# Kernel tuning notes

Hardware: AMD Instinct MI355X
Metric: run time of the kernel (lower is better)

The kernel has to match this reference:

```python
import jax, jax.numpy as jnp
import numpy as np

K = 3            # kernel_size
PAD = (K - 1) // 2
UM = 2           # um_dim
C_IN = 128
C_OUT = 128
SLOPE = 0.01     # F.leaky_relu default negative slope


def setup_inputs() -> dict:
    key = jax.random.key(0)
    k1, k2, k3 = jax.random.split(key, 3)
    xx = jax.random.normal(k1, (16, C_IN, 64, 64), dtype=jnp.float32)
    # Conv2d(C_in, C_out, K, stride=K, bias=True) parameters
    w = jax.random.normal(k2, (C_OUT, C_IN, K, K), dtype=jnp.float32) * 0.05
    b = jax.random.normal(k3, (C_OUT,), dtype=jnp.float32) * 0.05
    return {"xx": xx, "w": w, "b": b}


def reference(xx, w, b):
    B, C, H, Wd = xx.shape
    # --- unfold: replicate pad, then extract all KxK patches (stride 1) ---
    xp = jnp.pad(xx, ((0, 0), (0, 0), (PAD, PAD), (PAD, PAD)), mode="edge")
    # patches[b, c, r, s, i, j] = xp[b, c, i + r, j + s]   -> [B, C, K, K, H, W]
    patches = jnp.stack(
        [jnp.stack([xp[:, :, r:r + H, s:s + Wd] for s in range(K)], axis=2)
         for r in range(K)], axis=2)
    # --- subtract per-(um-slot, pixel) mean over channel groups and KxK ---
    g = patches.reshape(B, C // UM, UM, K, K, H, Wd)
    avgs = g.mean(axis=(1, 3, 4), keepdims=True)        # [B,1,UM,1,1,H,W]
    g = g - avgs
    p = g.reshape(B, C, K, K, H, Wd)
    # --- patch-wise conv (kernel_size == stride on the tiled image). The
    # torch code's transpose(2,4).transpose(-1,-2) tiling places patch col
    # offset s along tiled rows and row offset r along tiled cols, so the
    # conv weight w[o,c,r,s] pairs with patches[b,c,s,r,i,j]. ---
    out = jnp.einsum("ocrs,bcsrij->boij", w, p) + b[None, :, None, None]
    # leaky_relu
    out = jnp.where(out > 0, out, SLOPE * out)
    # --- add mean back per um-slot ---
    m = avgs[:, :, :, 0, 0]                             # [B,1,UM,H,W]
    O = out.shape[1]
    out = out.reshape(B, O // UM, UM, H, Wd) + m
    return out.reshape(B, O, H, Wd)
```

## Files before the change

kernel.cpp:

```cpp
#include <hip/hip_runtime.h>
#include <hip/hip_bf16.h>

typedef __bf16 bf16x8 __attribute__((ext_vector_type(8)));
typedef float  f32x4  __attribute__((ext_vector_type(4)));

#define NB 16
#define CI 128
#define CO 128
#define HH 64
#define WW 64

#define SROWS 4
#define SCOLS 66
#define SSTR  72

__global__ void prep(const float* __restrict__ w, __bf16* __restrict__ Ag,
                     float* __restrict__ wsum) {
    __shared__ float red[8];
    const int blk = blockIdx.x, tid = threadIdx.x;
    if (blk < 72) {
        int gid  = blk * 256 + tid;
        int l    = gid & 63;
        int frag = gid >> 6;
        int mt   = frag & 7;
        int t    = frag >> 3;
        int tap  = t >> 2;
        int r    = tap % 3;
        int s    = tap / 3;
        int o    = mt * 16 + (l & 15);
        int cb   = (t & 3) * 32 + (l >> 4) * 8;
        bf16x8 v;
        #pragma unroll
        for (int j = 0; j < 8; ++j)
            v[j] = (__bf16)w[((o * CI + cb + j) * 3 + r) * 3 + s];
        *(bf16x8*)(Ag + (size_t)gid * 8) = v;
    } else {
        int o = blk - 72;
        const float* p = w + (size_t)o * CI * 9;
        float se = 0.f, so = 0.f;
        for (int idx = tid; idx < CI * 9; idx += 256) {
            int c = idx / 9;
            float v = p[idx];
            if (c & 1) so += v; else se += v;
        }
        #pragma unroll
        for (int off = 32; off; off >>= 1) {
            se += __shfl_down(se, off);
            so += __shfl_down(so, off);
        }
        int wave = tid >> 6, lane = tid & 63;
        if (lane == 0) { red[wave * 2] = se; red[wave * 2 + 1] = so; }
        __syncthreads();
        if (tid == 0) {
            wsum[o]      = red[0] + red[2] + red[4] + red[6];
            wsum[CO + o] = red[1] + red[3] + red[5] + red[7];
        }
    }
}

__global__ __launch_bounds__(512, 4) void conv_main(
        const float* __restrict__ x,
        const float* __restrict__ bias,
        const float* __restrict__ wsum,
        const __bf16* __restrict__ Ag,
        float* __restrict__ out)
{
    __shared__ __align__(16) __bf16 slab[SROWS * SCOLS * SSTR];
    __shared__ float Srow[SROWS * SCOLS * 2];
    __shared__ float avgl[2 * 64 * 2];

    const int tid  = threadIdx.x;
    const int b    = blockIdx.y;
    const int row0 = blockIdx.x * 2;

    const float* xb = x + (size_t)b * CI * HH * WW;

    const int wave = tid >> 6, lane = tid & 63;
    const int wm = wave >> 1, wn = wave & 1;
    const int m = lane & 15, q = lane >> 4;

    f32x4 acc[2][4];
    #pragma unroll
    for (int i = 0; i < 2; ++i)
        #pragma unroll
        for (int j = 0; j < 4; ++j)
            acc[i][j] = (f32x4){0.f, 0.f, 0.f, 0.f};

    int bbase[4];
    #pragma unroll
    for (int nt = 0; nt < 4; ++nt)
        bbase[nt] = (wn * SCOLS + nt * 16 + m) * SSTR + q * 8;

    const __bf16* Aw = Ag + (size_t)(wm * 2) * 512 + (size_t)lane * 8;

    for (int half = 0; half < 2; ++half) {
        if (half) __syncthreads();
        for (int u = tid; u < SROWS * SCOLS * 8; u += 512) {
            int col = u % SCOLS;
            int rc  = u / SCOLS;
            int cg  = rc & 7;
            int r   = rc >> 3;
            int yi  = row0 - 1 + r; yi = yi < 0 ? 0 : (yi > HH - 1 ? HH - 1 : yi);
            int xi  = col - 1;      xi = xi < 0 ? 0 : (xi > WW - 1 ? WW - 1 : xi);
            const float* src = xb + (size_t)(half * 64 + cg * 8) * (HH * WW)
                                  + yi * WW + xi;
            bf16x8 v;
            #pragma unroll
            for (int j = 0; j < 8; ++j)
                v[j] = (__bf16)src[(size_t)j * (HH * WW)];
            *(bf16x8*)(slab + (r * SCOLS + col) * SSTR + cg * 8) = v;
        }
        __syncthreads();
        for (int u = tid; u < SROWS * SCOLS; u += 512) {
            const __bf16* p = slab + u * SSTR;
            float se = 0.f, so = 0.f;
            #pragma unroll
            for (int cg = 0; cg < 8; ++cg) {
                bf16x8 v = *(const bf16x8*)(p + cg * 8);
                se += (float)v[0] + (float)v[2] + (float)v[4] + (float)v[6];
                so += (float)v[1] + (float)v[3] + (float)v[5] + (float)v[7];
            }
            if (half) { se += Srow[u * 2 + 0]; so += Srow[u * 2 + 1]; }
            Srow[u * 2 + 0] = se;
            Srow[u * 2 + 1] = so;
        }
        __syncthreads();
        if (half == 1) {
            if (tid < 256) {
                int uu  = tid & 1;
                int col = (tid >> 1) & 63;
                int rr  = tid >> 7;
                float ssum = 0.f;
                #pragma unroll
                for (int dy = 0; dy < 3; ++dy)
                    #pragma unroll
                    for (int dx = 0; dx < 3; ++dx)
                        ssum += Srow[(((rr + dy) * SCOLS) + (col + dx)) * 2 + uu];
                avgl[tid] = ssum * (1.0f / 576.0f);
            }
            __syncthreads();
        }
        #pragma unroll
        for (int tap = 0; tap < 9; ++tap) {
            const int s_ = tap / 3, r3 = tap % 3;
            const int boff0 = (s_ * SCOLS + r3) * SSTR;
            #pragma unroll
            for (int cc = 0; cc < 2; ++cc) {
                const int t    = tap * 4 + half * 2 + cc;
                const int boff = boff0 + cc * 32;
                bf16x8 bfrag[4];
                #pragma unroll
                for (int nt = 0; nt < 4; ++nt)
                    bfrag[nt] = *(const bf16x8*)(slab + bbase[nt] + boff);
                bf16x8 afrag[2];
                #pragma unroll
                for (int i = 0; i < 2; ++i)
                    afrag[i] = *(const bf16x8*)(Aw + (size_t)t * 4096 + i * 512);
                #pragma unroll
                for (int i = 0; i < 2; ++i)
                    #pragma unroll
                    for (int nt = 0; nt < 4; ++nt)
                        acc[i][nt] = __builtin_amdgcn_mfma_f32_16x16x32_bf16(
                            afrag[i], bfrag[nt], acc[i][nt], 0, 0, 0);
            }
        }
    }

    float a0v[4], a1v[4];
    #pragma unroll
    for (int nt = 0; nt < 4; ++nt) {
        int col = nt * 16 + m;
        a0v[nt] = avgl[(wn * 64 + col) * 2 + 0];
        a1v[nt] = avgl[(wn * 64 + col) * 2 + 1];
    }
    float* outb = out + (size_t)b * CO * HH * WW + (size_t)(row0 + wn) * WW;
    #pragma unroll
    for (int i = 0; i < 2; ++i) {
        #pragma unroll
        for (int rg = 0; rg < 4; ++rg) {
            int o = wm * 32 + i * 16 + q * 4 + rg;
            float bo = bias[o];
            float w0 = wsum[o];
            float w1 = wsum[CO + o];
            float* po = outb + (size_t)o * (HH * WW);
            #pragma unroll
            for (int nt = 0; nt < 4; ++nt) {
                float v = acc[i][nt][rg] + bo - a0v[nt] * w0 - a1v[nt] * w1;
                v = v > 0.f ? v : 0.01f * v;
                v += (o & 1) ? a1v[nt] : a0v[nt];
                po[nt * 16 + m] = v;
            }
        }
    }
}

extern "C" void kernel_launch(void* const* d_in, const int* in_sizes, int n_in,
                              void* d_out, int out_size, void* d_ws, size_t ws_size,
                              hipStream_t stream) {
    const float* x    = (const float*)d_in[0];
    const float* w    = (const float*)d_in[1];
    const float* bias = (const float*)d_in[2];
    float* out = (float*)d_out;

    __bf16* Ag   = (__bf16*)d_ws;
    float*  wsum = (float*)((char*)d_ws + 294912);

    prep<<<200, 256, 0, stream>>>(w, Ag, wsum);

    dim3 grid(HH / 2, NB);
    conv_main<<<grid, 512, 0, stream>>>(x, bias, wsum, Ag, out);
}
```

Measured before the change: 104.6 us.

## Pre-transpose input to channel-quartered bf16, stage weights in LDS with async loads

```diff
diff --git a/kernel.cpp b/kernel.cpp
--- a/kernel.cpp
+++ b/kernel.cpp
@@ -10,16 +10,51 @@
 #define HH 64
 #define WW 64
 
-#define SROWS 4
 #define SCOLS 66
-#define SSTR  72
-
-__global__ void prep(const float* __restrict__ w, __bf16* __restrict__ Ag,
-                     float* __restrict__ wsum) {
+#define SPIX  (6 * SCOLS)
+#define QSZ   ((size_t)NB * HH * WW * 32)
+
+#define GLDS16(gp, lp) __builtin_amdgcn_global_load_lds( \
+    (const __attribute__((address_space(1))) unsigned int*)(const void*)(gp), \
+    (__attribute__((address_space(3))) unsigned int*)(void*)(lp), 16, 0, 0)
+
+__global__ void prep(const float* __restrict__ x, const float* __restrict__ w,
+                     __bf16* __restrict__ Ag, float* __restrict__ wsum,
+                     __bf16* __restrict__ xT, float* __restrict__ S) {
+    __shared__ float tile[128 * 65];
     __shared__ float red[8];
     const int blk = blockIdx.x, tid = threadIdx.x;
-    if (blk < 72) {
-        int gid  = blk * 256 + tid;
+    if (blk < 1024) {
+        const int bb = blk >> 6, y = blk & 63;
+        const float* xr = x + ((size_t)bb * CI) * (HH * WW) + y * WW;
+        for (int idx = tid; idx < 2048; idx += 256) {
+            int c = idx >> 4, x4 = idx & 15;
+            float4 v = *(const float4*)(xr + (size_t)c * (HH * WW) + x4 * 4);
+            *(float4*)(tile + c * 65 + x4 * 4) = v;
+        }
+        __syncthreads();
+        for (int idx = tid; idx < 1024; idx += 256) {
+            int px = idx >> 4, cg = idx & 15;
+            bf16x8 o8;
+            #pragma unroll
+            for (int j = 0; j < 8; ++j)
+                o8[j] = (__bf16)tile[(cg * 8 + j) * 65 + px];
+            __bf16* dst = xT + (size_t)(cg >> 2) * QSZ
+                        + (((size_t)bb * 64 + y) * 64 + px) * 32 + (cg & 3) * 8;
+            *(bf16x8*)dst = o8;
+        }
+        if (tid < 64) {
+            float se = 0.f, so = 0.f;
+            #pragma unroll 8
+            for (int c = 0; c < 128; c += 2) {
+                se += tile[c * 65 + tid];
+                so += tile[(c + 1) * 65 + tid];
+            }
+            float2 v = {se, so};
+            *(float2*)(S + (((size_t)bb * 64 + y) * 64 + tid) * 2) = v;
+        }
+    } else if (blk < 1096) {
+        int gid  = (blk - 1024) * 256 + tid;
         int l    = gid & 63;
         int frag = gid >> 6;
         int mt   = frag & 7;
@@ -35,7 +70,7 @@
             v[j] = (__bf16)w[((o * CI + cb + j) * 3 + r) * 3 + s];
         *(bf16x8*)(Ag + (size_t)gid * 8) = v;
     } else {
-        int o = blk - 72;
+        int o = blk - 1096;
         const float* p = w + (size_t)o * CI * 9;
         float se = 0.f, so = 0.f;
         for (int idx = tid; idx < CI * 9; idx += 256) {
@@ -48,8 +83,8 @@
             se += __shfl_down(se, off);
             so += __shfl_down(so, off);
         }
-        int wave = tid >> 6, lane = tid & 63;
-        if (lane == 0) { red[wave * 2] = se; red[wave * 2 + 1] = so; }
+        int wv = tid >> 6, lane = tid & 63;
+        if (lane == 0) { red[wv * 2] = se; red[wv * 2 + 1] = so; }
         __syncthreads();
         if (tid == 0) {
             wsum[o]      = red[0] + red[2] + red[4] + red[6];
@@ -58,30 +93,74 @@
     }
 }
 
-__global__ __launch_bounds__(512, 4) void conv_main(
-        const float* __restrict__ x,
+__global__ __launch_bounds__(512, 2) void conv_main(
+        const __bf16* __restrict__ xT,
+        const float* __restrict__ S,
         const float* __restrict__ bias,
         const float* __restrict__ wsum,
         const __bf16* __restrict__ Ag,
         float* __restrict__ out)
 {
-    __shared__ __align__(16) __bf16 slab[SROWS * SCOLS * SSTR];
-    __shared__ float Srow[SROWS * SCOLS * 2];
-    __shared__ float avgl[2 * 64 * 2];
+    __shared__ __align__(16) __bf16 Alds[9 * 4096];
+    __shared__ __align__(16) __bf16 slab[2][SPIX * 32];
+    __shared__ float SrowS[6 * 64 * 2];
+    __shared__ float avgl[512];
 
     const int tid  = threadIdx.x;
     const int b    = blockIdx.y;
-    const int row0 = blockIdx.x * 2;
-
-    const float* xb = x + (size_t)b * CI * HH * WW;
+    const int row0 = blockIdx.x * 4;
 
     const int wave = tid >> 6, lane = tid & 63;
-    const int wm = wave >> 1, wn = wave & 1;
-    const int m = lane & 15, q = lane >> 4;
-
-    f32x4 acc[2][4];
-    #pragma unroll
-    for (int i = 0; i < 2; ++i)
+    const int wm = wave >> 2;
+    const int wn = wave & 3;
+    const int m = lane & 15, qv = lane >> 4;
+
+    auto issue_A = [&](int qn, int a0, int a1) {
+        for (int a = a0 + wave; a < a1; a += 8) {
+            int tap = a >> 3, part = a & 7;
+            const __bf16* gp = Ag
+                + (((size_t)((tap * 4 + qn) * 8 + part)) << 9) + (lane << 3);
+            GLDS16(gp, &Alds[(size_t)a << 9]);
+        }
+    };
+    auto issue_slab = [&](int qn, __bf16* dst) {
+        for (int c = wave; c < 25; c += 8) {
+            int p   = c * 16 + (lane >> 2);
+            int r   = (p * 993) >> 16;
+            int col = p - r * 66;
+            int yi  = row0 - 1 + r; yi = yi < 0 ? 0 : (yi > 63 ? 63 : yi);
+            int xi  = col - 1;      xi = xi < 0 ? 0 : (xi > 63 ? 63 : xi);
+            const __bf16* gp = xT + (size_t)qn * QSZ
+                + (((size_t)b * 64 + yi) * 64 + xi) * 32 + (lane & 3) * 8;
+            if (p < SPIX) GLDS16(gp, dst + ((size_t)c << 9));
+        }
+    };
+
+    issue_slab(0, slab[0]);
+    issue_A(0, 0, 72);
+    for (int idx = tid; idx < 768; idx += 512) {
+        int r = idx >> 7, rem = idx & 127;
+        int col = rem >> 1, uu = idx & 1;
+        int yi = row0 - 1 + r; yi = yi < 0 ? 0 : (yi > 63 ? 63 : yi);
+        SrowS[idx] = S[(((size_t)b * 64 + yi) * 64 + col) * 2 + uu];
+    }
+    __syncthreads();
+    {
+        int rr = tid >> 7, col = (tid >> 1) & 63, uu = tid & 1;
+        float ssum = 0.f;
+        #pragma unroll
+        for (int dy = 0; dy < 3; ++dy)
+            #pragma unroll
+            for (int dx = 0; dx < 3; ++dx) {
+                int cc = col - 1 + dx; cc = cc < 0 ? 0 : (cc > 63 ? 63 : cc);
+                ssum += SrowS[((rr + dy) * 64 + cc) * 2 + uu];
+            }
+        avgl[tid] = ssum * (1.0f / 576.0f);
+    }
+
+    f32x4 acc[4][4];
+    #pragma unroll
+    for (int i = 0; i < 4; ++i)
         #pragma unroll
         for (int j = 0; j < 4; ++j)
             acc[i][j] = (f32x4){0.f, 0.f, 0.f, 0.f};
@@ -89,96 +168,67 @@
     int bbase[4];
     #pragma unroll
     for (int nt = 0; nt < 4; ++nt)
-        bbase[nt] = (wn * SCOLS + nt * 16 + m) * SSTR + q * 8;
-
-    const __bf16* Aw = Ag + (size_t)(wm * 2) * 512 + (size_t)lane * 8;
-
-    for (int half = 0; half < 2; ++half) {
-        if (half) __syncthreads();
-        for (int u = tid; u < SROWS * SCOLS * 8; u += 512) {
-            int col = u % SCOLS;
-            int rc  = u / SCOLS;
-            int cg  = rc & 7;
-            int r   = rc >> 3;
-            int yi  = row0 - 1 + r; yi = yi < 0 ? 0 : (yi > HH - 1 ? HH - 1 : yi);
-            int xi  = col - 1;      xi = xi < 0 ? 0 : (xi > WW - 1 ? WW - 1 : xi);
-            const float* src = xb + (size_t)(half * 64 + cg * 8) * (HH * WW)
-                                  + yi * WW + xi;
-            bf16x8 v;
-            #pragma unroll
-            for (int j = 0; j < 8; ++j)
-                v[j] = (__bf16)src[(size_t)j * (HH * WW)];
-            *(bf16x8*)(slab + (r * SCOLS + col) * SSTR + cg * 8) = v;
-        }
-        __syncthreads();
-        for (int u = tid; u < SROWS * SCOLS; u += 512) {
-            const __bf16* p = slab + u * SSTR;
-            float se = 0.f, so = 0.f;
-            #pragma unroll
-            for (int cg = 0; cg < 8; ++cg) {
-                bf16x8 v = *(const bf16x8*)(p + cg * 8);
-                se += (float)v[0] + (float)v[2] + (float)v[4] + (float)v[6];
-                so += (float)v[1] + (float)v[3] + (float)v[5] + (float)v[7];
-            }
-            if (half) { se += Srow[u * 2 + 0]; so += Srow[u * 2 + 1]; }
-            Srow[u * 2 + 0] = se;
-            Srow[u * 2 + 1] = so;
-        }
-        __syncthreads();
-        if (half == 1) {
-            if (tid < 256) {
-                int uu  = tid & 1;
-                int col = (tid >> 1) & 63;
-                int rr  = tid >> 7;
-                float ssum = 0.f;
-                #pragma unroll
-                for (int dy = 0; dy < 3; ++dy)
-                    #pragma unroll
-                    for (int dx = 0; dx < 3; ++dx)
-                        ssum += Srow[(((rr + dy) * SCOLS) + (col + dx)) * 2 + uu];
-                avgl[tid] = ssum * (1.0f / 576.0f);
-            }
-            __syncthreads();
-        }
-        #pragma unroll
-        for (int tap = 0; tap < 9; ++tap) {
+        bbase[nt] = (wn * SCOLS + nt * 16 + m) * 32 + qv * 8;
+    const __bf16* Aw = Alds + (wm * 4) * 512 + lane * 8;
+
+    for (int q = 0; q < 4; ++q) {
+        const __bf16* sl = slab[q & 1];
+        if (q < 3) issue_slab(q + 1, slab[(q + 1) & 1]);
+        #pragma unroll
+        for (int tap = 0; tap < 4; ++tap) {
             const int s_ = tap / 3, r3 = tap % 3;
-            const int boff0 = (s_ * SCOLS + r3) * SSTR;
-            #pragma unroll
-            for (int cc = 0; cc < 2; ++cc) {
-                const int t    = tap * 4 + half * 2 + cc;
-                const int boff = boff0 + cc * 32;
-                bf16x8 bfrag[4];
+            const int poff = (s_ * SCOLS + r3) * 32;
+            bf16x8 Bf[4], Af[4];
+            #pragma unroll
+            for (int nt = 0; nt < 4; ++nt)
+                Bf[nt] = *(const bf16x8*)(sl + bbase[nt] + poff);
+            #pragma unroll
+            for (int i = 0; i < 4; ++i)
+                Af[i] = *(const bf16x8*)(Aw + (tap * 8 + i) * 512);
+            #pragma unroll
+            for (int i = 0; i < 4; ++i)
                 #pragma unroll
                 for (int nt = 0; nt < 4; ++nt)
-                    bfrag[nt] = *(const bf16x8*)(slab + bbase[nt] + boff);
-                bf16x8 afrag[2];
+                    acc[i][nt] = __builtin_amdgcn_mfma_f32_16x16x32_bf16(
+                        Af[i], Bf[nt], acc[i][nt], 0, 0, 0);
+        }
+        __syncthreads();
+        if (q < 3) issue_A(q + 1, 0, 32);
+        #pragma unroll
+        for (int tap = 4; tap < 9; ++tap) {
+            const int s_ = tap / 3, r3 = tap % 3;
+            const int poff = (s_ * SCOLS + r3) * 32;
+            bf16x8 Bf[4], Af[4];
+            #pragma unroll
+            for (int nt = 0; nt < 4; ++nt)
+                Bf[nt] = *(const bf16x8*)(sl + bbase[nt] + poff);
+            #pragma unroll
+            for (int i = 0; i < 4; ++i)
+                Af[i] = *(const bf16x8*)(Aw + (tap * 8 + i) * 512);
+            #pragma unroll
+            for (int i = 0; i < 4; ++i)
                 #pragma unroll
-                for (int i = 0; i < 2; ++i)
-                    afrag[i] = *(const bf16x8*)(Aw + (size_t)t * 4096 + i * 512);
-                #pragma unroll
-                for (int i = 0; i < 2; ++i)
-                    #pragma unroll
-                    for (int nt = 0; nt < 4; ++nt)
-                        acc[i][nt] = __builtin_amdgcn_mfma_f32_16x16x32_bf16(
-                            afrag[i], bfrag[nt], acc[i][nt], 0, 0, 0);
-            }
-        }
+                for (int nt = 0; nt < 4; ++nt)
+                    acc[i][nt] = __builtin_amdgcn_mfma_f32_16x16x32_bf16(
+                        Af[i], Bf[nt], acc[i][nt], 0, 0, 0);
+        }
+        __syncthreads();
+        if (q < 3) issue_A(q + 1, 32, 72);
     }
 
     float a0v[4], a1v[4];
     #pragma unroll
     for (int nt = 0; nt < 4; ++nt) {
         int col = nt * 16 + m;
-        a0v[nt] = avgl[(wn * 64 + col) * 2 + 0];
-        a1v[nt] = avgl[(wn * 64 + col) * 2 + 1];
+        a0v[nt] = avgl[wn * 128 + col * 2 + 0];
+        a1v[nt] = avgl[wn * 128 + col * 2 + 1];
     }
     float* outb = out + (size_t)b * CO * HH * WW + (size_t)(row0 + wn) * WW;
     #pragma unroll
-    for (int i = 0; i < 2; ++i) {
+    for (int i = 0; i < 4; ++i) {
         #pragma unroll
         for (int rg = 0; rg < 4; ++rg) {
-            int o = wm * 32 + i * 16 + q * 4 + rg;
+            int o = wm * 64 + i * 16 + qv * 4 + rg;
             float bo = bias[o];
             float w0 = wsum[o];
             float w1 = wsum[CO + o];
@@ -188,7 +238,7 @@
                 float v = acc[i][nt][rg] + bo - a0v[nt] * w0 - a1v[nt] * w1;
                 v = v > 0.f ? v : 0.01f * v;
                 v += (o & 1) ? a1v[nt] : a0v[nt];
-                po[nt * 16 + m] = v;
+                __builtin_nontemporal_store(v, po + nt * 16 + m);
             }
         }
     }
@@ -204,9 +254,11 @@
 
     __bf16* Ag   = (__bf16*)d_ws;
     float*  wsum = (float*)((char*)d_ws + 294912);
-
-    prep<<<200, 256, 0, stream>>>(w, Ag, wsum);
-
-    dim3 grid(HH / 2, NB);
-    conv_main<<<grid, 512, 0, stream>>>(x, bias, wsum, Ag, out);
+    __bf16* xT   = (__bf16*)((char*)d_ws + 295936);
+    float*  S    = (float*)((char*)d_ws + 295936 + 2 * QSZ * 4);
+
+    prep<<<1224, 256, 0, stream>>>(x, w, Ag, wsum, xT, S);
+
+    dim3 grid(HH / 4, NB);
+    conv_main<<<grid, 512, 0, stream>>>(xT, S, bias, wsum, Ag, out);
 }
```

After: 113.1 us. 8.1% more time.
